# Kernel tuning notes

Measured on AMD Instinct MI355X. Metric: run time of the kernel, lower is better.

The kernel has to match this reference:

```python
import jax, jax.numpy as jnp
import numpy as np

N_CHO, N_JUNG, N_JONG = 19, 21, 28
N_COMPS = N_CHO + N_JUNG + N_JONG  # 68
N_STYLES = 32
B = 512
C, H, W = 128, 16, 16


def setup_inputs() -> dict:
    key = jax.random.key(0)
    ks = jax.random.split(key, 8)
    style_ids = jax.random.randint(ks[0], (B,), 0, N_STYLES, dtype=jnp.int64 if jax.config.jax_enable_x64 else jnp.int32)
    comp_ids = jax.random.randint(ks[1], (B, 3), 0, N_CHO, dtype=style_ids.dtype)  # valid for all 3 cols (19<=21,28)
    comp_feats = jax.random.normal(ks[2], (B, 3, C, H, W), dtype=jnp.float32)
    bias = jax.random.normal(ks[3], (N_COMPS, C, H, W), dtype=jnp.float32)
    fan = C * 9
    w1 = jax.random.normal(ks[4], (C, C, 3, 3), jnp.float32) / np.sqrt(fan)
    w2 = jax.random.normal(ks[5], (C, C, 3, 3), jnp.float32) / np.sqrt(fan)
    w3 = jax.random.normal(ks[6], (C, C, 3, 3), jnp.float32) / np.sqrt(fan)
    b1 = jnp.zeros((C,), jnp.float32)
    b2 = jnp.zeros((C,), jnp.float32)
    b3 = jnp.zeros((C,), jnp.float32)
    return {"style_ids": style_ids, "comp_ids": comp_ids, "comp_feats": comp_feats,
            "bias": bias, "w1": w1, "b1": b1, "w2": w2, "b2": b2, "w3": w3, "b3": b3}


def _conv_relu(x, w, b):
    # ConvBlock: 3x3 conv, pad 1, + ReLU (dmfont ConvBlock)
    y = jax.lax.conv_general_dilated(x, w, (1, 1), 'SAME',
                                     dimension_numbers=('NCHW', 'OIHW', 'NCHW'))
    return jax.nn.relu(y + b[None, :, None, None])


def reference(style_ids, comp_ids, comp_feats, bias, w1, b1, w2, b2, w3, b3):
    # comp_id_to_addr (kor): offset columns by [0, N_CHO, N_CHO+N_JUNG]
    offsets = jnp.array([0, N_CHO, N_CHO + N_JUNG], dtype=comp_ids.dtype)
    addrs = comp_ids + offsets[None, :]                       # [B, 3]
    keys = (style_ids[:, None] * N_COMPS + addrs).reshape(-1)  # [B*3]

    # DynamicMemory.write + read(reduction='mean') == scatter-mean by (style, addr) key
    feats = comp_feats.reshape(B * 3, C, H, W)
    nseg = N_STYLES * N_COMPS
    sums = jax.ops.segment_sum(feats, keys, num_segments=nseg)           # [nseg, C, H, W]
    cnts = jax.ops.segment_sum(jnp.ones((B * 3,), feats.dtype), keys, num_segments=nseg)
    means = sums / jnp.maximum(cnts, 1.0)[:, None, None, None]
    mem = means[keys].reshape(B, 3, C, H, W)

    # PersistentMemory: gather bias by addr, run 3-block conv hypernet, add
    pb = bias[addrs.reshape(-1)]                              # [B*3, C, H, W]
    pb = _conv_relu(pb, w1, b1)
    pb = _conv_relu(pb, w2, b2)
    pb = _conv_relu(pb, w3, b3)
    return mem + pb.reshape(B, 3, C, H, W)
```

## Files before the change

### kernel.cpp

```cpp
#include <hip/hip_runtime.h>

typedef __attribute__((ext_vector_type(8))) unsigned short ushort8_t;
typedef __attribute__((ext_vector_type(8))) __bf16 bf16x8;
typedef __attribute__((ext_vector_type(16))) float f32x16;

#define NSEG 2176
#define NITEM 1536

__device__ inline unsigned short f2bf(float f) {
    unsigned int b = __builtin_bit_cast(unsigned int, f);
    b += 0x7FFFu + ((b >> 16) & 1u);
    return (unsigned short)(b >> 16);
}
__device__ inline float bf2f(unsigned short h) {
    unsigned int b = ((unsigned int)h) << 16;
    return __builtin_bit_cast(float, b);
}

__global__ __launch_bounds__(256) void kA(const int* __restrict__ style,
                                          const int* __restrict__ cids,
                                          int* __restrict__ addr_g, int* __restrict__ key_g,
                                          int* __restrict__ rank_g, int* __restrict__ list_g,
                                          int* __restrict__ segstart_g, int* __restrict__ segcnt_g) {
    __shared__ int cnt[NSEG];
    __shared__ int sstart[NSEG];
    __shared__ int partial[256];
    const int tid = threadIdx.x;
    for (int s = tid; s < NSEG; s += 256) cnt[s] = 0;
    __syncthreads();
    int myrank[6], mykey[6];
    #pragma unroll
    for (int k = 0; k < 6; ++k) {
        const int i = k * 256 + tid;
        const int b = i / 3, j = i - b * 3;
        const int off = (j == 0) ? 0 : (j == 1) ? 19 : 40;
        const int a = cids[i] + off;
        const int key = style[b] * 68 + a;
        addr_g[i] = a; key_g[i] = key;
        mykey[k] = key;
        myrank[k] = atomicAdd(&cnt[key], 1);
        rank_g[i] = myrank[k];
    }
    __syncthreads();
    const int base = tid * 9;
    int ssum = 0;
    for (int q = 0; q < 9; ++q) { int s = base + q; if (s < NSEG) ssum += cnt[s]; }
    partial[tid] = ssum;
    __syncthreads();
    if (tid == 0) {
        int run = 0;
        for (int t = 0; t < 256; ++t) { int tmp = partial[t]; partial[t] = run; run += tmp; }
    }
    __syncthreads();
    int run = partial[tid];
    for (int q = 0; q < 9; ++q) {
        int s = base + q;
        if (s < NSEG) { sstart[s] = run; segstart_g[s] = run; segcnt_g[s] = cnt[s]; run += cnt[s]; }
    }
    __syncthreads();
    #pragma unroll
    for (int k = 0; k < 6; ++k) {
        const int i = k * 256 + tid;
        list_g[sstart[mykey[k]] + myrank[k]] = i;
    }
}

__global__ __launch_bounds__(256) void kW(const float* __restrict__ w1,
                                          const float* __restrict__ w2,
                                          const float* __restrict__ w3,
                                          unsigned short* __restrict__ Bp) {
    const int t = blockIdx.x * 256 + threadIdx.x;
    if (t >= 3 * 147456) return;
    const int l = t / 147456;
    const int o = t - l * 147456;
    const int slot = o & 7;
    const int co = (o >> 3) & 127;
    const int kb = o >> 10;
    const int tap = kb >> 4;
    const int ci = ((kb & 15) << 3) | slot;
    const float* w = (l == 0) ? w1 : (l == 1) ? w2 : w3;
    Bp[t] = f2bf(w[(co * 128 + ci) * 9 + tap]);
}

__global__ __launch_bounds__(256) void kConv(const float* __restrict__ bias_in,
                                             const unsigned short* __restrict__ inter_in,
                                             const unsigned short* __restrict__ Bp,
                                             const float* __restrict__ bvec,
                                             unsigned short* __restrict__ inter_out,
                                             unsigned short* __restrict__ pbu_out,
                                             int layer) {
    extern __shared__ char lds[];
    const int tid = threadIdx.x;
    const int u = blockIdx.x;

    if (layer == 0) {
        const float* src = bias_in + (size_t)u * 32768;
        const int m = tid;
        const int swz = (m & 15) << 4;
        #pragma unroll 4
        for (int c = 0; c < 128; ++c) {
            const float v = src[c * 256 + m];
            const int off = (m * 256 + c * 2) ^ swz;
            *(unsigned short*)(lds + off) = f2bf(v);
        }
    } else {
        const uint4* src = (const uint4*)(inter_in + (size_t)u * 32768);
        uint4* dst = (uint4*)lds;
        #pragma unroll
        for (int r = 0; r < 16; ++r) dst[r * 256 + tid] = src[r * 256 + tid];
    }
    __syncthreads();

    const int lane = tid & 63;
    const int wid = tid >> 6;
    const int wm = wid >> 1;
    const int wn = wid & 1;
    const int lrow = lane & 31;
    const int lhi = lane >> 5;

    f32x16 acc[4][2] = {};

    for (int kk = 0; kk < 72; ++kk) {
        const int tap = kk >> 3;
        const int oh = tap / 3 - 1;
        const int ow = tap % 3 - 1;
        const int ci0 = (kk & 7) * 16 + lhi * 8;
        const int kb = kk * 2 + lhi;

        bf16x8 bfrag[2];
        #pragma unroll
        for (int t2 = 0; t2 < 2; ++t2) {
            const int co = (wn * 2 + t2) * 32 + lrow;
            bfrag[t2] = __builtin_bit_cast(bf16x8,
                *(const ushort8_t*)(Bp + ((size_t)(kb * 128 + co)) * 8));
        }
        bf16x8 afrag[4];
        #pragma unroll
        for (int t = 0; t < 4; ++t) {
            const int m = (wm * 4 + t) * 32 + lrow;
            const int h = (m >> 4) + oh;
            const int w = (m & 15) + ow;
            ushort8_t v = {0, 0, 0, 0, 0, 0, 0, 0};
            if ((unsigned)h < 16u && (unsigned)w < 16u) {
                const int m2 = h * 16 + w;
                const int off = (m2 * 256 + ci0 * 2) ^ ((m2 & 15) << 4);
                v = *(const ushort8_t*)(lds + off);
            }
            afrag[t] = __builtin_bit_cast(bf16x8, v);
        }
        #pragma unroll
        for (int t = 0; t < 4; ++t)
            #pragma unroll
            for (int t2 = 0; t2 < 2; ++t2)
                acc[t][t2] = __builtin_amdgcn_mfma_f32_32x32x16_bf16(
                    afrag[t], bfrag[t2], acc[t][t2], 0, 0, 0);
    }

    #pragma unroll
    for (int t2 = 0; t2 < 2; ++t2) {
        const int co = (wn * 2 + t2) * 32 + lrow;
        const float bb = bvec[co];
        #pragma unroll
        for (int t = 0; t < 4; ++t) {
            const int tmb = (wm * 4 + t) * 32;
            if (layer < 2) {
                #pragma unroll
                for (int r = 0; r < 16; ++r) {
                    const int m = tmb + (r & 3) + 8 * (r >> 2) + 4 * lhi;
                    const float v = fmaxf(acc[t][t2][r] + bb, 0.0f);
                    const int off = (m * 256 + co * 2) ^ ((m & 15) << 4);
                    *(unsigned short*)((char*)inter_out + (size_t)u * 65536 + off) = f2bf(v);
                }
            } else {
                #pragma unroll
                for (int rq = 0; rq < 4; ++rq) {
                    const int m0 = tmb + 8 * rq + 4 * lhi;
                    ushort4 pk;
                    pk.x = f2bf(fmaxf(acc[t][t2][rq * 4 + 0] + bb, 0.0f));
                    pk.y = f2bf(fmaxf(acc[t][t2][rq * 4 + 1] + bb, 0.0f));
                    pk.z = f2bf(fmaxf(acc[t][t2][rq * 4 + 2] + bb, 0.0f));
                    pk.w = f2bf(fmaxf(acc[t][t2][rq * 4 + 3] + bb, 0.0f));
                    *(ushort4*)(pbu_out + (size_t)u * 32768 + co * 256 + m0) = pk;
                }
            }
        }
    }
}

__global__ __launch_bounds__(256) void kB(const float* __restrict__ feats,
                                          const unsigned short* __restrict__ pbu,
                                          const int* __restrict__ addr_g,
                                          const int* __restrict__ key_g,
                                          const int* __restrict__ rank_g,
                                          const int* __restrict__ list_g,
                                          const int* __restrict__ segstart_g,
                                          const int* __restrict__ segcnt_g,
                                          float* __restrict__ out) {
    const int i = blockIdx.y;
    if (rank_g[i] != 0) return;
    const int s = key_g[i];
    const int st = segstart_g[s];
    const int n = segcnt_g[s];
    const int e = blockIdx.x * 1024 + threadIdx.x * 4;
    float sx = 0.f, sy = 0.f, sz = 0.f, sw = 0.f;
    for (int t = 0; t < n; ++t) {
        const int j = list_g[st + t];
        const float4 v = *(const float4*)(feats + (size_t)j * 32768 + e);
        sx += v.x; sy += v.y; sz += v.z; sw += v.w;
    }
    const float inv = 1.0f / (float)n;
    sx *= inv; sy *= inv; sz *= inv; sw *= inv;
    for (int t = 0; t < n; ++t) {
        const int j = list_g[st + t];
        const int a = addr_g[j];
        const ushort4 p = *(const ushort4*)(pbu + (size_t)a * 32768 + e);
        float4 o;
        o.x = sx + bf2f(p.x);
        o.y = sy + bf2f(p.y);
        o.z = sz + bf2f(p.z);
        o.w = sw + bf2f(p.w);
        *(float4*)(out + (size_t)j * 32768 + e) = o;
    }
}

extern "C" void kernel_launch(void* const* d_in, const int* in_sizes, int n_in,
                              void* d_out, int out_size, void* d_ws, size_t ws_size,
                              hipStream_t stream) {
    const int* style   = (const int*)d_in[0];
    const int* cids    = (const int*)d_in[1];
    const float* feats = (const float*)d_in[2];
    const float* bias  = (const float*)d_in[3];
    const float* w1    = (const float*)d_in[4];
    const float* b1    = (const float*)d_in[5];
    const float* w2    = (const float*)d_in[6];
    const float* b2    = (const float*)d_in[7];
    const float* w3    = (const float*)d_in[8];
    const float* b3    = (const float*)d_in[9];
    float* out = (float*)d_out;
    char* ws = (char*)d_ws;

    int* addr_g     = (int*)(ws + 0);
    int* key_g      = (int*)(ws + 6144);
    int* rank_g     = (int*)(ws + 12288);
    int* list_g     = (int*)(ws + 18432);
    int* segstart_g = (int*)(ws + 24576);
    int* segcnt_g   = (int*)(ws + 33280);
    unsigned short* Bp     = (unsigned short*)(ws + 65536);
    unsigned short* interA = (unsigned short*)(ws + 1048576);
    unsigned short* interB = (unsigned short*)(ws + 5505024);
    unsigned short* pbu    = (unsigned short*)(ws + 9961472);

    hipLaunchKernelGGL(kA, dim3(1), dim3(256), 0, stream,
                       style, cids, addr_g, key_g, rank_g, list_g, segstart_g, segcnt_g);
    hipLaunchKernelGGL(kW, dim3(1728), dim3(256), 0, stream, w1, w2, w3, Bp);
    hipLaunchKernelGGL(kConv, dim3(68), dim3(256), 65536, stream,
                       bias, (const unsigned short*)nullptr, Bp, b1, interA,
                       (unsigned short*)nullptr, 0);
    hipLaunchKernelGGL(kConv, dim3(68), dim3(256), 65536, stream,
                       (const float*)nullptr, interA, Bp + 147456, b2, interB,
                       (unsigned short*)nullptr, 1);
    hipLaunchKernelGGL(kConv, dim3(68), dim3(256), 65536, stream,
                       (const float*)nullptr, interB, Bp + 2 * 147456, b3,
                       (unsigned short*)nullptr, pbu, 2);
    hipLaunchKernelGGL(kB, dim3(32, NITEM), dim3(256), 0, stream,
                       feats, pbu, addr_g, key_g, rank_g, list_g, segstart_g, segcnt_g, out);
}
```

Before: 460.7 us.

## Fuse three conv layers into one kernel with LDS-resident activations

Merges the three per-layer conv launches into a single 512-thread kernel per component. The intermediate activations stay in LDS between layers instead of round-tripping through global memory. Each wave now computes a 2x2 tile of 32x32 MFMA blocks rather than 4x2, and the loop is unrolled by 2. The serial 256-element prefix scan in kA is also replaced by a wave shuffle scan. The grid stays at 68 blocks, so most CUs sit idle, and the extra barriers between layers add synchronisation in exchange for removing two launches and the global traffic.

```diff
diff --git a/kernel.cpp b/kernel.cpp
--- a/kernel.cpp
+++ b/kernel.cpp
@@ -26,6 +26,8 @@
     __shared__ int sstart[NSEG];
     __shared__ int partial[256];
     const int tid = threadIdx.x;
+    const int lane = tid & 63;
+    const int wid = tid >> 6;
     for (int s = tid; s < NSEG; s += 256) cnt[s] = 0;
     __syncthreads();
     int myrank[6], mykey[6];
@@ -47,9 +49,21 @@
     for (int q = 0; q < 9; ++q) { int s = base + q; if (s < NSEG) ssum += cnt[s]; }
     partial[tid] = ssum;
     __syncthreads();
-    if (tid == 0) {
-        int run = 0;
-        for (int t = 0; t < 256; ++t) { int tmp = partial[t]; partial[t] = run; run += tmp; }
+    if (wid == 0) {
+        int s0 = partial[lane * 4 + 0], s1 = partial[lane * 4 + 1];
+        int s2 = partial[lane * 4 + 2], s3 = partial[lane * 4 + 3];
+        const int loc = s0 + s1 + s2 + s3;
+        int pre = loc;
+        #pragma unroll
+        for (int d = 1; d < 64; d <<= 1) {
+            const int o = __shfl_up(pre, d);
+            if (lane >= d) pre += o;
+        }
+        pre -= loc;
+        partial[lane * 4 + 0] = pre;
+        partial[lane * 4 + 1] = pre + s0;
+        partial[lane * 4 + 2] = pre + s0 + s1;
+        partial[lane * 4 + 3] = pre + s0 + s1 + s2;
     }
     __syncthreads();
     int run = partial[tid];
@@ -82,32 +96,27 @@
     Bp[t] = f2bf(w[(co * 128 + ci) * 9 + tap]);
 }
 
-__global__ __launch_bounds__(256) void kConv(const float* __restrict__ bias_in,
-                                             const unsigned short* __restrict__ inter_in,
-                                             const unsigned short* __restrict__ Bp,
-                                             const float* __restrict__ bvec,
-                                             unsigned short* __restrict__ inter_out,
-                                             unsigned short* __restrict__ pbu_out,
-                                             int layer) {
-    extern __shared__ char lds[];
+__global__ __launch_bounds__(512) void kConvF(const float* __restrict__ bias_in,
+                                              const unsigned short* __restrict__ Bp,
+                                              const float* __restrict__ b1,
+                                              const float* __restrict__ b2,
+                                              const float* __restrict__ b3,
+                                              unsigned short* __restrict__ pbu_out) {
+    __shared__ char lds[65536];
     const int tid = threadIdx.x;
     const int u = blockIdx.x;
 
-    if (layer == 0) {
+    {
         const float* src = bias_in + (size_t)u * 32768;
-        const int m = tid;
+        const int m = tid & 255;
+        const int c0 = (tid >> 8) * 64;
         const int swz = (m & 15) << 4;
         #pragma unroll 4
-        for (int c = 0; c < 128; ++c) {
+        for (int c = c0; c < c0 + 64; ++c) {
             const float v = src[c * 256 + m];
             const int off = (m * 256 + c * 2) ^ swz;
             *(unsigned short*)(lds + off) = f2bf(v);
         }
-    } else {
-        const uint4* src = (const uint4*)(inter_in + (size_t)u * 32768);
-        uint4* dst = (uint4*)lds;
-        #pragma unroll
-        for (int r = 0; r < 16; ++r) dst[r * 256 + tid] = src[r * 256 + tid];
     }
     __syncthreads();
 
@@ -118,69 +127,94 @@
     const int lrow = lane & 31;
     const int lhi = lane >> 5;
 
-    f32x16 acc[4][2] = {};
-
-    for (int kk = 0; kk < 72; ++kk) {
-        const int tap = kk >> 3;
-        const int oh = tap / 3 - 1;
-        const int ow = tap % 3 - 1;
-        const int ci0 = (kk & 7) * 16 + lhi * 8;
-        const int kb = kk * 2 + lhi;
-
-        bf16x8 bfrag[2];
-        #pragma unroll
-        for (int t2 = 0; t2 < 2; ++t2) {
-            const int co = (wn * 2 + t2) * 32 + lrow;
-            bfrag[t2] = __builtin_bit_cast(bf16x8,
-                *(const ushort8_t*)(Bp + ((size_t)(kb * 128 + co)) * 8));
-        }
-        bf16x8 afrag[4];
-        #pragma unroll
-        for (int t = 0; t < 4; ++t) {
-            const int m = (wm * 4 + t) * 32 + lrow;
-            const int h = (m >> 4) + oh;
-            const int w = (m & 15) + ow;
-            ushort8_t v = {0, 0, 0, 0, 0, 0, 0, 0};
-            if ((unsigned)h < 16u && (unsigned)w < 16u) {
-                const int m2 = h * 16 + w;
-                const int off = (m2 * 256 + ci0 * 2) ^ ((m2 & 15) << 4);
-                v = *(const ushort8_t*)(lds + off);
+    for (int layer = 0; layer < 3; ++layer) {
+        const unsigned short* Bpl = Bp + (size_t)layer * 147456;
+        const float* bv = (layer == 0) ? b1 : (layer == 1) ? b2 : b3;
+
+        f32x16 acc[2][2] = {};
+
+        #pragma unroll 2
+        for (int kk = 0; kk < 72; ++kk) {
+            const int tap = kk >> 3;
+            const int t3 = tap / 3;
+            const int oh = t3 - 1;
+            const int ow = (tap - t3 * 3) - 1;
+            const int ci0 = (kk & 7) * 16 + lhi * 8;
+            const int kb = kk * 2 + lhi;
+
+            bf16x8 bfrag[2];
+            #pragma unroll
+            for (int t2 = 0; t2 < 2; ++t2) {
+                const int co = (wn * 2 + t2) * 32 + lrow;
+                bfrag[t2] = __builtin_bit_cast(bf16x8,
+                    *(const ushort8_t*)(Bpl + ((size_t)(kb * 128 + co)) * 8));
             }
-            afrag[t] = __builtin_bit_cast(bf16x8, v);
-        }
-        #pragma unroll
-        for (int t = 0; t < 4; ++t)
-            #pragma unroll
-            for (int t2 = 0; t2 < 2; ++t2)
-                acc[t][t2] = __builtin_amdgcn_mfma_f32_32x32x16_bf16(
-                    afrag[t], bfrag[t2], acc[t][t2], 0, 0, 0);
-    }
-
-    #pragma unroll
-    for (int t2 = 0; t2 < 2; ++t2) {
-        const int co = (wn * 2 + t2) * 32 + lrow;
-        const float bb = bvec[co];
-        #pragma unroll
-        for (int t = 0; t < 4; ++t) {
-            const int tmb = (wm * 4 + t) * 32;
-            if (layer < 2) {
-                #pragma unroll
-                for (int r = 0; r < 16; ++r) {
-                    const int m = tmb + (r & 3) + 8 * (r >> 2) + 4 * lhi;
-                    const float v = fmaxf(acc[t][t2][r] + bb, 0.0f);
-                    const int off = (m * 256 + co * 2) ^ ((m & 15) << 4);
-                    *(unsigned short*)((char*)inter_out + (size_t)u * 65536 + off) = f2bf(v);
-                }
-            } else {
-                #pragma unroll
-                for (int rq = 0; rq < 4; ++rq) {
-                    const int m0 = tmb + 8 * rq + 4 * lhi;
-                    ushort4 pk;
-                    pk.x = f2bf(fmaxf(acc[t][t2][rq * 4 + 0] + bb, 0.0f));
-                    pk.y = f2bf(fmaxf(acc[t][t2][rq * 4 + 1] + bb, 0.0f));
-                    pk.z = f2bf(fmaxf(acc[t][t2][rq * 4 + 2] + bb, 0.0f));
-                    pk.w = f2bf(fmaxf(acc[t][t2][rq * 4 + 3] + bb, 0.0f));
-                    *(ushort4*)(pbu_out + (size_t)u * 32768 + co * 256 + m0) = pk;
+            bf16x8 afrag[2];
+            #pragma unroll
+            for (int t = 0; t < 2; ++t) {
+                const int m = (wm * 2 + t) * 32 + lrow;
+                const int h = (m >> 4) + oh;
+                const int w = (m & 15) + ow;
+                ushort8_t v = {0, 0, 0, 0, 0, 0, 0, 0};
+                if ((unsigned)h < 16u && (unsigned)w < 16u) {
+                    const int m2 = h * 16 + w;
+                    const int off = (m2 * 256 + ci0 * 2) ^ ((m2 & 15) << 4);
+                    v = *(const ushort8_t*)(lds + off);
+                }
+                afrag[t] = __builtin_bit_cast(bf16x8, v);
+            }
+            #pragma unroll
+            for (int t = 0; t < 2; ++t)
+                #pragma unroll
+                for (int t2 = 0; t2 < 2; ++t2)
+                    acc[t][t2] = __builtin_amdgcn_mfma_f32_32x32x16_bf16(
+                        afrag[t], bfrag[t2], acc[t][t2], 0, 0, 0);
+        }
+
+        if (layer < 2) {
+            unsigned short pk[2][2][16];
+            #pragma unroll
+            for (int t = 0; t < 2; ++t)
+                #pragma unroll
+                for (int t2 = 0; t2 < 2; ++t2) {
+                    const int co = (wn * 2 + t2) * 32 + lrow;
+                    const float bb = bv[co];
+                    #pragma unroll
+                    for (int r = 0; r < 16; ++r)
+                        pk[t][t2][r] = f2bf(fmaxf(acc[t][t2][r] + bb, 0.0f));
+                }
+            __syncthreads();
+            #pragma unroll
+            for (int t = 0; t < 2; ++t)
+                #pragma unroll
+                for (int t2 = 0; t2 < 2; ++t2) {
+                    const int co = (wn * 2 + t2) * 32 + lrow;
+                    #pragma unroll
+                    for (int r = 0; r < 16; ++r) {
+                        const int m = (wm * 2 + t) * 32 + (r & 3) + 8 * (r >> 2) + 4 * lhi;
+                        const int off = (m * 256 + co * 2) ^ ((m & 15) << 4);
+                        *(unsigned short*)(lds + off) = pk[t][t2][r];
+                    }
+                }
+            __syncthreads();
+        } else {
+            #pragma unroll
+            for (int t2 = 0; t2 < 2; ++t2) {
+                const int co = (wn * 2 + t2) * 32 + lrow;
+                const float bb = bv[co];
+                #pragma unroll
+                for (int t = 0; t < 2; ++t) {
+                    const int tmb = (wm * 2 + t) * 32;
+                    #pragma unroll
+                    for (int rq = 0; rq < 4; ++rq) {
+                        const int m0 = tmb + 8 * rq + 4 * lhi;
+                        ushort4 pkv;
+                        pkv.x = f2bf(fmaxf(acc[t][t2][rq * 4 + 0] + bb, 0.0f));
+                        pkv.y = f2bf(fmaxf(acc[t][t2][rq * 4 + 1] + bb, 0.0f));
+                        pkv.z = f2bf(fmaxf(acc[t][t2][rq * 4 + 2] + bb, 0.0f));
+                        pkv.w = f2bf(fmaxf(acc[t][t2][rq * 4 + 3] + bb, 0.0f));
+                        *(ushort4*)(pbu_out + (size_t)u * 32768 + co * 256 + m0) = pkv;
+                    }
                 }
             }
         }
@@ -245,23 +279,14 @@
     int* list_g     = (int*)(ws + 18432);
     int* segstart_g = (int*)(ws + 24576);
     int* segcnt_g   = (int*)(ws + 33280);
-    unsigned short* Bp     = (unsigned short*)(ws + 65536);
-    unsigned short* interA = (unsigned short*)(ws + 1048576);
-    unsigned short* interB = (unsigned short*)(ws + 5505024);
-    unsigned short* pbu    = (unsigned short*)(ws + 9961472);
+    unsigned short* Bp  = (unsigned short*)(ws + 65536);
+    unsigned short* pbu = (unsigned short*)(ws + 1048576);
 
     hipLaunchKernelGGL(kA, dim3(1), dim3(256), 0, stream,
                        style, cids, addr_g, key_g, rank_g, list_g, segstart_g, segcnt_g);
     hipLaunchKernelGGL(kW, dim3(1728), dim3(256), 0, stream, w1, w2, w3, Bp);
-    hipLaunchKernelGGL(kConv, dim3(68), dim3(256), 65536, stream,
-                       bias, (const unsigned short*)nullptr, Bp, b1, interA,
-                       (unsigned short*)nullptr, 0);
-    hipLaunchKernelGGL(kConv, dim3(68), dim3(256), 65536, stream,
-                       (const float*)nullptr, interA, Bp + 147456, b2, interB,
-                       (unsigned short*)nullptr, 1);
-    hipLaunchKernelGGL(kConv, dim3(68), dim3(256), 65536, stream,
-                       (const float*)nullptr, interB, Bp + 2 * 147456, b3,
-                       (unsigned short*)nullptr, pbu, 2);
+    hipLaunchKernelGGL(kConvF, dim3(68), dim3(512), 0, stream,
+                       bias, Bp, b1, b2, b3, pbu);
     hipLaunchKernelGGL(kB, dim3(32, NITEM), dim3(256), 0, stream,
                        feats, pbu, addr_g, key_g, rank_g, list_g, segstart_g, segcnt_g, out);
 }
```

Measured after the change: 431.1 us. -6.4%, faster.
